# Performance work log

Hardware: AMD Instinct MI355X
Metric: run time of the kernel (lower is better)

Reference implementation:

```python
import jax, jax.numpy as jnp
import numpy as np

H = W = 2048
TANH_C = 1.1486328125  # probability-correction constant from the model
DEG2RAD = np.float32(np.pi / 180.0)

# Fire-spread direction angle (degrees, East=0, counterclockwise) from the
# neighbor at 3x3 window position (r, c) toward the center cell.
DIR_DEG = jnp.array([[315., 270., 225.],
                     [  0.,   0., 180.],
                     [ 45.,  90., 135.]], dtype=jnp.float32)
CENTER_MASK = jnp.ones((3, 3), jnp.float32).at[1, 1].set(0.0)  # exclude self


def _neighborhood(x):
    """x: [H,W] -> [H,W,3,3] with [i,j,r,c] = x[i+r-1, j+c-1], zero padded."""
    xp = jnp.pad(x, 1)
    return jnp.stack(
        [jnp.stack([xp[r:r + H, c:c + W] for c in range(3)], axis=-1)
         for r in range(3)], axis=-2)


def setup_inputs() -> dict:
    key = jax.random.key(0)
    ks = jax.random.split(key, 8)
    p_veg = jax.random.uniform(ks[0], (H, W), jnp.float32)
    p_den = jax.random.uniform(ks[1], (H, W), jnp.float32)
    wind_velocity = jax.random.uniform(ks[2], (H, W), jnp.float32) * 10.0
    wind_towards_direction = jax.random.uniform(ks[3], (H, W), jnp.float32) * 360.0
    slope = (jax.random.uniform(ks[4], (H, W, 3, 3), jnp.float32) - 0.5) * 60.0
    burning = jax.random.uniform(ks[5], (H, W)) < 0.01  # sparse initial ignition
    burned = jnp.zeros((H, W), dtype=bool)
    rand_ignite = jax.random.uniform(ks[6], (H, W), jnp.float32)
    rand_continue = jax.random.uniform(ks[7], (H, W), jnp.float32)
    return dict(
        p_veg=p_veg, p_den=p_den,
        wind_velocity=wind_velocity, wind_towards_direction=wind_towards_direction,
        slope=slope,
        a=jnp.float32(0.1), p_h=jnp.float32(0.3),
        c_1=jnp.float32(0.1), c_2=jnp.float32(0.1), p_continue=jnp.float32(0.3),
        rand_ignite=rand_ignite, rand_continue=rand_continue,
        burning=burning, burned=burned,
    )


def reference(p_veg, p_den, wind_velocity, wind_towards_direction, slope,
              a, p_h, c_1, c_2, p_continue,
              rand_ignite, rand_continue, burning, burned):
    # p_w = exp(c1*V) * exp(c2*V*(cos(theta_w)-1)), theta_w = angle between
    # wind direction and per-neighbor spread direction. [H,W,3,3]
    theta_w = (wind_towards_direction[..., None, None] - DIR_DEG) * DEG2RAD
    p_w = (jnp.exp(c_1 * wind_velocity)[..., None, None]
           * jnp.exp(c_2 * wind_velocity[..., None, None] * (jnp.cos(theta_w) - 1.0)))
    # p_s = exp(a * theta_s), slope angle in radians. [H,W,3,3]
    p_s = jnp.exp(a * slope * DEG2RAD)
    # p_propagate = tanh(c * p_h*(1+p_veg)*(1+p_den)*p_w*p_s)
    p_base = p_h * (1.0 + p_veg) * (1.0 + p_den)  # [H,W]
    p_prop = jnp.tanh(TANH_C * (p_base[..., None, None] * p_w * p_s))
    # 8-neighbor burning indicators (center masked out). [H,W,3,3]
    nbr_burning = _neighborhood(burning.astype(jnp.float32)) * CENTER_MASK
    # p_ignite = 1 - prod_j (1 - p_propagate_j * burning_j)
    p_ignite = 1.0 - jnp.prod(1.0 - p_prop * nbr_burning, axis=(-2, -1))
    # Stochastic state transition.
    burnable = ~burning & ~burned
    new_ignited = burnable & (rand_ignite < p_ignite)
    keep = burning & (rand_continue < p_continue)
    new_burning = new_ignited | keep
    new_burned = burned | (burning & ~keep)
    return p_ignite, jnp.stack([new_burning, new_burned])
```

## Files before the change

### kernel.cpp

```cpp
#include <hip/hip_runtime.h>
#include <math.h>

namespace {

constexpr int H = 2048;
constexpr int W = 2048;
constexpr float TANH_C  = 1.1486328125f;
constexpr float DEG2RAD = 0.017453292519943295f;
constexpr float RT2H    = 0.70710678118654752f;
constexpr float LOG2E   = 1.4426950408889634f;
constexpr float TWOPI   = 6.283185307179586f;

__device__ __forceinline__ float fexp2(float x) {
#if __has_builtin(__builtin_amdgcn_exp2f)
    return __builtin_amdgcn_exp2f(x);
#else
    return __exp2f(x);
#endif
}
__device__ __forceinline__ float fcos_rev(float x) {
#if __has_builtin(__builtin_amdgcn_cosf)
    return __builtin_amdgcn_cosf(x);
#else
    return __cosf(x * TWOPI);
#endif
}
__device__ __forceinline__ float fsin_rev(float x) {
#if __has_builtin(__builtin_amdgcn_sinf)
    return __builtin_amdgcn_sinf(x);
#else
    return __sinf(x * TWOPI);
#endif
}
__device__ __forceinline__ float frcp(float x) {
#if __has_builtin(__builtin_amdgcn_rcpf)
    return __builtin_amdgcn_rcpf(x);
#else
    return 1.0f / x;
#endif
}

__global__ __launch_bounds__(256) void wildfire_step(
    const float* __restrict__ p_veg,  const float* __restrict__ p_den,
    const float* __restrict__ wind_v, const float* __restrict__ wind_d,
    const float* __restrict__ slope,
    const float* __restrict__ s_a,  const float* __restrict__ s_ph,
    const float* __restrict__ s_c1, const float* __restrict__ s_c2,
    const float* __restrict__ s_pc,
    const float* __restrict__ rand_ig, const float* __restrict__ rand_co,
    const int* __restrict__ burning, const int* __restrict__ burned,
    float* __restrict__ out)
{
    __shared__ float sb[3][260];
    const int t  = (int)threadIdx.x;
    const int i  = (int)blockIdx.y;
    const int j0 = (int)blockIdx.x * 256;
    const int j  = j0 + t;

    for (int r = 0; r < 3; ++r) {
        const int ii = i + r - 1;
        for (int c = t; c < 258; c += 256) {
            const int jj = j0 - 1 + c;
            float v = 0.f;
            if (ii >= 0 && ii < H && jj >= 0 && jj < W)
                v = burning[ii * W + jj] ? 1.f : 0.f;
            sb[r][c] = v;
        }
    }
    __syncthreads();

    const float b0 = sb[0][t], b1 = sb[0][t+1], b2 = sb[0][t+2];
    const float b3 = sb[1][t], bc = sb[1][t+1], b5 = sb[1][t+2];
    const float b6 = sb[2][t], b7 = sb[2][t+1], b8 = sb[2][t+2];

    const int   idx        = i * W + j;
    const bool  is_burning = (bc != 0.f);
    const int   was_burned = burned[idx];
    const float rco        = rand_co[idx];
    const float p_cont     = s_pc[0];
    const float a    = s_a[0];
    const float p_h  = s_ph[0];
    const float c1   = s_c1[0];
    const float c2   = s_c2[0];

    const float any_n = ((b0 + b1) + (b2 + b3)) + ((b5 + b6) + (b7 + b8));

    float p_ignite    = 0.f;
    bool  new_ignited = false;

    if (any_n != 0.f) {
        const float pv  = p_veg[idx];
        const float pd  = p_den[idx];
        const float wv  = wind_v[idx];
        const float wd  = wind_d[idx];
        const float rig = rand_ig[idx];
        const float* sp = slope + (size_t)idx * 9;
        const float sl0 = sp[0], sl1 = sp[1], sl2 = sp[2];
        const float sl3 = sp[3], sl5 = sp[5];
        const float sl6 = sp[6], sl7 = sp[7], sl8 = sp[8];

        const float wrev = wd * (1.f / 360.f);
        const float cw = fcos_rev(wrev);
        const float sw = fsin_rev(wrev);

        const float Lc2wv = (LOG2E * c2) * wv;
        const float cwv = Lc2wv * cw, swv = Lc2wv * sw;
        const float cwr = RT2H * cwv, swr = RT2H * swv;
        const float dpl = cwr + swr;
        const float dmi = cwr - swr;
        const float aslL = (a * DEG2RAD) * LOG2E;
        const float p_base = (p_h * (1.f + pv)) * (1.f + pd);
        const float Cz2 = (2.f * LOG2E * TANH_C) * p_base
                        * fexp2(LOG2E * (c1 * wv - c2 * wv));

#define NEIGHBOR(K, b, T, sl)                                            \
        const float q##K = fmaf(aslL, (sl), (T));                        \
        const float z##K = Cz2 * fexp2(q##K);                            \
        const float E##K = fexp2(z##K);                                  \
        const float d##K = fmaf((b), E##K, 1.f);

        NEIGHBOR(0, b0,  dmi, sl0)
        NEIGHBOR(1, b1, -swv, sl1)
        NEIGHBOR(2, b2, -dpl, sl2)
        NEIGHBOR(3, b3,  cwv, sl3)
        NEIGHBOR(5, b5, -cwv, sl5)
        NEIGHBOR(6, b6,  dpl, sl6)
        NEIGHBOR(7, b7,  swv, sl7)
        NEIGHBOR(8, b8, -dmi, sl8)
#undef NEIGHBOR
        const float den = ((d0 * d1) * (d2 * d3)) * ((d5 * d6) * (d7 * d8));
        const float num = fexp2(any_n);
        p_ignite = fmaf(-num, frcp(den), 1.f);

        new_ignited = (!is_burning) && (was_burned == 0) && (rig < p_ignite);
    }

    const bool keep = is_burning && (rco < p_cont);
    const bool nb   = new_ignited || keep;
    const bool nd   = (was_burned != 0) || (is_burning && !keep);

    out[idx]             = p_ignite;
    out[H * W + idx]     = nb ? 1.f : 0.f;
    out[2 * H * W + idx] = nd ? 1.f : 0.f;
}

}

extern "C" void kernel_launch(void* const* d_in, const int* in_sizes, int n_in,
                              void* d_out, int out_size, void* d_ws, size_t ws_size,
                              hipStream_t stream)
{
    (void)in_sizes; (void)n_in; (void)out_size; (void)d_ws; (void)ws_size;
    dim3 grid(W / 256, H, 1);
    dim3 block(256, 1, 1);
    hipLaunchKernelGGL(wildfire_step, grid, block, 0, stream,
        (const float*)d_in[0],  (const float*)d_in[1],
        (const float*)d_in[2],  (const float*)d_in[3],
        (const float*)d_in[4],
        (const float*)d_in[5],  (const float*)d_in[6],
        (const float*)d_in[7],  (const float*)d_in[8],
        (const float*)d_in[9],
        (const float*)d_in[10], (const float*)d_in[11],
        (const int*)d_in[12],   (const int*)d_in[13],
        (float*)d_out);
}
```

Baseline: 306.2 us.

## Process four pixels per thread with vectorized loads and stores

```diff
diff --git a/kernel.cpp b/kernel.cpp
--- a/kernel.cpp
+++ b/kernel.cpp
@@ -5,6 +5,7 @@
 
 constexpr int H = 2048;
 constexpr int W = 2048;
+constexpr int HW = H * W;
 constexpr float TANH_C  = 1.1486328125f;
 constexpr float DEG2RAD = 0.017453292519943295f;
 constexpr float RT2H    = 0.70710678118654752f;
@@ -51,15 +52,14 @@
     const int* __restrict__ burning, const int* __restrict__ burned,
     float* __restrict__ out)
 {
-    __shared__ float sb[3][260];
+    __shared__ __align__(16) float sb[3][1032];
     const int t  = (int)threadIdx.x;
     const int i  = (int)blockIdx.y;
-    const int j0 = (int)blockIdx.x * 256;
-    const int j  = j0 + t;
+    const int j0 = (int)blockIdx.x * 1024;
 
     for (int r = 0; r < 3; ++r) {
         const int ii = i + r - 1;
-        for (int c = t; c < 258; c += 256) {
+        for (int c = t; c < 1026; c += 256) {
             const int jj = j0 - 1 + c;
             float v = 0.f;
             if (ii >= 0 && ii < H && jj >= 0 && jj < W)
@@ -69,79 +69,120 @@
     }
     __syncthreads();
 
-    const float b0 = sb[0][t], b1 = sb[0][t+1], b2 = sb[0][t+2];
-    const float b3 = sb[1][t], bc = sb[1][t+1], b5 = sb[1][t+2];
-    const float b6 = sb[2][t], b7 = sb[2][t+1], b8 = sb[2][t+2];
-
-    const int   idx        = i * W + j;
-    const bool  is_burning = (bc != 0.f);
-    const int   was_burned = burned[idx];
-    const float rco        = rand_co[idx];
-    const float p_cont     = s_pc[0];
-    const float a    = s_a[0];
-    const float p_h  = s_ph[0];
-    const float c1   = s_c1[0];
-    const float c2   = s_c2[0];
-
-    const float any_n = ((b0 + b1) + (b2 + b3)) + ((b5 + b6) + (b7 + b8));
-
-    float p_ignite    = 0.f;
-    bool  new_ignited = false;
-
-    if (any_n != 0.f) {
-        const float pv  = p_veg[idx];
-        const float pd  = p_den[idx];
-        const float wv  = wind_v[idx];
-        const float wd  = wind_d[idx];
-        const float rig = rand_ig[idx];
-        const float* sp = slope + (size_t)idx * 9;
-        const float sl0 = sp[0], sl1 = sp[1], sl2 = sp[2];
-        const float sl3 = sp[3], sl5 = sp[5];
-        const float sl6 = sp[6], sl7 = sp[7], sl8 = sp[8];
-
-        const float wrev = wd * (1.f / 360.f);
-        const float cw = fcos_rev(wrev);
-        const float sw = fsin_rev(wrev);
-
-        const float Lc2wv = (LOG2E * c2) * wv;
-        const float cwv = Lc2wv * cw, swv = Lc2wv * sw;
-        const float cwr = RT2H * cwv, swr = RT2H * swv;
-        const float dpl = cwr + swr;
-        const float dmi = cwr - swr;
-        const float aslL = (a * DEG2RAD) * LOG2E;
-        const float p_base = (p_h * (1.f + pv)) * (1.f + pd);
-        const float Cz2 = (2.f * LOG2E * TANH_C) * p_base
-                        * fexp2(LOG2E * (c1 * wv - c2 * wv));
-
-#define NEIGHBOR(K, b, T, sl)                                            \
-        const float q##K = fmaf(aslL, (sl), (T));                        \
-        const float z##K = Cz2 * fexp2(q##K);                            \
-        const float E##K = fexp2(z##K);                                  \
-        const float d##K = fmaf((b), E##K, 1.f);
-
-        NEIGHBOR(0, b0,  dmi, sl0)
-        NEIGHBOR(1, b1, -swv, sl1)
-        NEIGHBOR(2, b2, -dpl, sl2)
-        NEIGHBOR(3, b3,  cwv, sl3)
-        NEIGHBOR(5, b5, -cwv, sl5)
-        NEIGHBOR(6, b6,  dpl, sl6)
-        NEIGHBOR(7, b7,  swv, sl7)
-        NEIGHBOR(8, b8, -dmi, sl8)
+    const int jb  = t * 4;
+    const int idx = i * W + j0 + jb;
+
+    float r0[8], r1[8], r2[8];
+    {
+        const float4 a0 = *reinterpret_cast<const float4*>(&sb[0][jb]);
+        const float4 a1 = *reinterpret_cast<const float4*>(&sb[0][jb + 4]);
+        const float4 b0 = *reinterpret_cast<const float4*>(&sb[1][jb]);
+        const float4 b1 = *reinterpret_cast<const float4*>(&sb[1][jb + 4]);
+        const float4 c0 = *reinterpret_cast<const float4*>(&sb[2][jb]);
+        const float4 c1 = *reinterpret_cast<const float4*>(&sb[2][jb + 4]);
+        r0[0]=a0.x; r0[1]=a0.y; r0[2]=a0.z; r0[3]=a0.w; r0[4]=a1.x; r0[5]=a1.y; r0[6]=a1.z; r0[7]=a1.w;
+        r1[0]=b0.x; r1[1]=b0.y; r1[2]=b0.z; r1[3]=b0.w; r1[4]=b1.x; r1[5]=b1.y; r1[6]=b1.z; r1[7]=b1.w;
+        r2[0]=c0.x; r2[1]=c0.y; r2[2]=c0.z; r2[3]=c0.w; r2[4]=c1.x; r2[5]=c1.y; r2[6]=c1.z; r2[7]=c1.w;
+    }
+
+    float anyn[4], pig[4];
+    bool  isb[4], ni[4];
+#pragma unroll
+    for (int x = 0; x < 4; ++x) {
+        anyn[x] = ((r0[x] + r0[x+1]) + (r0[x+2] + r1[x]))
+                + ((r1[x+2] + r2[x]) + (r2[x+1] + r2[x+2]));
+        isb[x]  = (r1[x+1] != 0.f);
+        pig[x]  = 0.f;
+        ni[x]   = false;
+    }
+
+    const int4  burned4 = *reinterpret_cast<const int4*>(burned + idx);
+    const int   bn[4]   = {burned4.x, burned4.y, burned4.z, burned4.w};
+    const float p_cont  = s_pc[0];
+
+    float rc[4] = {0.f, 0.f, 0.f, 0.f};
+    if (isb[0] || isb[1] || isb[2] || isb[3]) {
+        const float4 rco4 = *reinterpret_cast<const float4*>(rand_co + idx);
+        rc[0]=rco4.x; rc[1]=rco4.y; rc[2]=rco4.z; rc[3]=rco4.w;
+    }
+
+    if ((anyn[0] + anyn[1] + anyn[2] + anyn[3]) != 0.f) {
+        const float a_  = s_a[0];
+        const float p_h = s_ph[0];
+        const float c1  = s_c1[0];
+        const float c2  = s_c2[0];
+
+        const float4 pv4  = *reinterpret_cast<const float4*>(p_veg  + idx);
+        const float4 pd4  = *reinterpret_cast<const float4*>(p_den  + idx);
+        const float4 wv4  = *reinterpret_cast<const float4*>(wind_v + idx);
+        const float4 wd4  = *reinterpret_cast<const float4*>(wind_d + idx);
+        const float4 rig4 = *reinterpret_cast<const float4*>(rand_ig + idx);
+        const float pv[4]  = {pv4.x, pv4.y, pv4.z, pv4.w};
+        const float pd[4]  = {pd4.x, pd4.y, pd4.z, pd4.w};
+        const float wv[4]  = {wv4.x, wv4.y, wv4.z, wv4.w};
+        const float wd[4]  = {wd4.x, wd4.y, wd4.z, wd4.w};
+        const float rig[4] = {rig4.x, rig4.y, rig4.z, rig4.w};
+
+        float sl[36];
+        __builtin_memcpy(sl, slope + (size_t)idx * 9, 36 * sizeof(float));
+
+        const float aslL = (a_ * DEG2RAD) * LOG2E;
+
+#pragma unroll
+        for (int x = 0; x < 4; ++x) {
+            if (anyn[x] != 0.f) {
+                const float wrev = wd[x] * (1.f / 360.f);
+                const float cw = fcos_rev(wrev);
+                const float sw = fsin_rev(wrev);
+
+                const float Lc2wv = (LOG2E * c2) * wv[x];
+                const float cwv = Lc2wv * cw, swv = Lc2wv * sw;
+                const float cwr = RT2H * cwv, swr = RT2H * swv;
+                const float dpl = cwr + swr;
+                const float dmi = cwr - swr;
+                const float p_base = (p_h * (1.f + pv[x])) * (1.f + pd[x]);
+                const float Cz2 = (2.f * LOG2E * TANH_C) * p_base
+                                * fexp2(LOG2E * (c1 * wv[x] - c2 * wv[x]));
+                const float* s = sl + 9 * x;
+
+#define NEIGHBOR(K, b, T, sv)                                            \
+                const float q##K = fmaf(aslL, (sv), (T));                \
+                const float z##K = Cz2 * fexp2(q##K);                    \
+                const float E##K = fexp2(z##K);                          \
+                const float d##K = fmaf((b), E##K, 1.f);
+
+                NEIGHBOR(0, r0[x],    dmi, s[0])
+                NEIGHBOR(1, r0[x+1], -swv, s[1])
+                NEIGHBOR(2, r0[x+2], -dpl, s[2])
+                NEIGHBOR(3, r1[x],    cwv, s[3])
+                NEIGHBOR(5, r1[x+2], -cwv, s[5])
+                NEIGHBOR(6, r2[x],    dpl, s[6])
+                NEIGHBOR(7, r2[x+1],  swv, s[7])
+                NEIGHBOR(8, r2[x+2], -dmi, s[8])
 #undef NEIGHBOR
-        const float den = ((d0 * d1) * (d2 * d3)) * ((d5 * d6) * (d7 * d8));
-        const float num = fexp2(any_n);
-        p_ignite = fmaf(-num, frcp(den), 1.f);
-
-        new_ignited = (!is_burning) && (was_burned == 0) && (rig < p_ignite);
-    }
-
-    const bool keep = is_burning && (rco < p_cont);
-    const bool nb   = new_ignited || keep;
-    const bool nd   = (was_burned != 0) || (is_burning && !keep);
-
-    out[idx]             = p_ignite;
-    out[H * W + idx]     = nb ? 1.f : 0.f;
-    out[2 * H * W + idx] = nd ? 1.f : 0.f;
+                const float den = ((d0 * d1) * (d2 * d3)) * ((d5 * d6) * (d7 * d8));
+                const float num = fexp2(anyn[x]);
+                pig[x] = fmaf(-num, frcp(den), 1.f);
+
+                ni[x] = (!isb[x]) && (bn[x] == 0) && (rig[x] < pig[x]);
+            }
+        }
+    }
+
+    float4 o0, o1, o2;
+    float* o0p = &o0.x; float* o1p = &o1.x; float* o2p = &o2.x;
+#pragma unroll
+    for (int x = 0; x < 4; ++x) {
+        const bool keep = isb[x] && (rc[x] < p_cont);
+        const bool nb   = ni[x] || keep;
+        const bool nd   = (bn[x] != 0) || (isb[x] && !keep);
+        o0p[x] = pig[x];
+        o1p[x] = nb ? 1.f : 0.f;
+        o2p[x] = nd ? 1.f : 0.f;
+    }
+    *reinterpret_cast<float4*>(out + idx)          = o0;
+    *reinterpret_cast<float4*>(out + HW + idx)     = o1;
+    *reinterpret_cast<float4*>(out + 2 * HW + idx) = o2;
 }
 
 }
@@ -151,7 +192,7 @@
                               hipStream_t stream)
 {
     (void)in_sizes; (void)n_in; (void)out_size; (void)d_ws; (void)ws_size;
-    dim3 grid(W / 256, H, 1);
+    dim3 grid(W / 1024, H, 1);
     dim3 block(256, 1, 1);
     hipLaunchKernelGGL(wildfire_step, grid, block, 0, stream,
         (const float*)d_in[0],  (const float*)d_in[1],
```

Result: slower. 317.7 us (+3.7%).
